# Kernel optimization log

Measured on AMD Instinct MI355X. Metric: run time of the kernel, lower is better.

The kernel has to match this reference:

```python
import jax, jax.numpy as jnp
import numpy as np

SOS = 1  # from init_kwargs

def gru_cell(x, h, W_ih, W_hh, b_ih, b_hh):
    # torch nn.GRU single-step cell semantics
    gi = x @ W_ih.T + b_ih            # [B, 3H]
    gh = h @ W_hh.T + b_hh            # [B, 3H]
    i_r, i_z, i_n = jnp.split(gi, 3, axis=-1)
    h_r, h_z, h_n = jnp.split(gh, 3, axis=-1)
    r = jax.nn.sigmoid(i_r + h_r)
    z = jax.nn.sigmoid(i_z + h_z)
    n = jnp.tanh(i_n + r * h_n)
    return (1.0 - z) * n + z * h

def setup_inputs() -> dict:
    key = jax.random.key(0)
    ks = jax.random.split(key, 12)
    V, E, H, L, B = 32000, 512, 512, 2, 32
    s = lambda k, shape: (jax.random.normal(k, shape, jnp.float32) * 0.05)
    return dict(
        h_0=s(ks[0], (L, B, H)),
        emb=s(ks[1], (V, E)),
        W_ih0=s(ks[2], (3 * H, E)), W_hh0=s(ks[3], (3 * H, H)),
        b_ih0=s(ks[4], (3 * H,)),   b_hh0=s(ks[5], (3 * H,)),
        W_ih1=s(ks[6], (3 * H, H)), W_hh1=s(ks[7], (3 * H, H)),
        b_ih1=s(ks[8], (3 * H,)),   b_hh1=s(ks[9], (3 * H,)),
        W_out=s(ks[10], (V, H)),    b_out=s(ks[11], (V,)),
        max_n=64,
    )

def reference(h_0, emb, W_ih0, W_hh0, b_ih0, b_hh0,
              W_ih1, W_hh1, b_ih1, b_hh1, W_out, b_out, max_n):
    B = h_0.shape[1]
    tok0 = jnp.full((B,), SOS, dtype=jnp.int32)

    def step(carry, _):
        h, tok = carry                              # h: [2, B, H], tok: [B]
        x = emb[tok]                                # [B, E] embedding gather
        h0n = gru_cell(x,   h[0], W_ih0, W_hh0, b_ih0, b_hh0)
        h1n = gru_cell(h0n, h[1], W_ih1, W_hh1, b_ih1, b_hh1)
        logits = h1n @ W_out.T + b_out              # [B, V]
        ntok = jnp.argmax(logits, axis=-1).astype(jnp.int32)
        return (jnp.stack([h0n, h1n]), ntok), ntok

    (h_t, _), toks = jax.lax.scan(step, (h_0, tok0), None, length=max_n)
    # toks: [max_n, B] -> [B, max_n] to mirror per-sequence output lists
    return toks.T, h_t
```

## Files before the change

kernel.cpp:

```cpp
#include <hip/hip_runtime.h>
#include <math.h>

#define NBLK 256
#define NTHR 512
#define Bsz  32
#define Hsz  512
#define Vsz  32000
#define BH   (Bsz*Hsz)
#define LDP  516
#define LDPB 520
#define CBLK 250
#define EPS  0.0045f

#define WS_HBUF   0
#define WS_PACKED 131072
#define WS_PLB    135168
#define WS_BAR    139264
#define WS_WPACK  143360
#define WS_WNORM  32911360
#define WS_CBAR   33039360
#define WS_NEEDED 33043456

#define PACKED_SEED 0x00000000FFFFFFFEull

typedef short short8 __attribute__((ext_vector_type(8)));
typedef float f32x4  __attribute__((ext_vector_type(4)));

struct Args {
  const float* h0_init;
  const float* emb;
  const float* Wih0; const float* Whh0; const float* bih0; const float* bhh0;
  const float* Wih1; const float* Whh1; const float* bih1; const float* bhh1;
  const float* Wout; const float* bout;
  const int*   maxn;
  float* out;
  float* hbuf;
  unsigned long long* packed;
  unsigned* plb;
  unsigned* bar;
  unsigned* cbar;
  const unsigned* wpack;
  const float* wnormE;
};

__device__ __forceinline__ unsigned short bf16_rne(float f){
  unsigned u = __float_as_uint(f);
  unsigned r = u + 0x7FFFu + ((u >> 16) & 1u);
  return (unsigned short)(r >> 16);
}
__device__ __forceinline__ float bf16v(float f){
  unsigned u = ((unsigned)bf16_rne(f)) << 16;
  return __uint_as_float(u);
}
__device__ __forceinline__ unsigned key32(float f){
  unsigned u = __float_as_uint(f);
  return (u & 0x80000000u) ? ~u : (u | 0x80000000u);
}

__device__ __forceinline__ unsigned long long cload8(const void* p){
  return __hip_atomic_load((const unsigned long long*)p,
                           __ATOMIC_RELAXED, __HIP_MEMORY_SCOPE_AGENT);
}
__device__ __forceinline__ unsigned cload4u(const unsigned* p){
  return __hip_atomic_load(p, __ATOMIC_RELAXED, __HIP_MEMORY_SCOPE_AGENT);
}
__device__ __forceinline__ void cstore4(float* p, float v){
  __hip_atomic_store(p, v, __ATOMIC_RELAXED, __HIP_MEMORY_SCOPE_AGENT);
}
__device__ __forceinline__ void cstore4u(unsigned* p, unsigned v){
  __hip_atomic_store(p, v, __ATOMIC_RELAXED, __HIP_MEMORY_SCOPE_AGENT);
}
__device__ __forceinline__ void cstore8(void* p, unsigned long long v){
  __hip_atomic_store((unsigned long long*)p, v,
                     __ATOMIC_RELAXED, __HIP_MEMORY_SCOPE_AGENT);
}

__device__ __forceinline__ short8 ntload8(const void* p){
  return __builtin_nontemporal_load((const short8*)p);
}

__device__ __forceinline__ void gridbar(unsigned* bar, int bid){
  __syncthreads();
  if (threadIdx.x == 0){
    asm volatile("s_waitcnt vmcnt(0)" ::: "memory");
    const int g = bid & 7;
    unsigned* gcnt = bar + g*32;
    unsigned* root = bar + 8*32;
    unsigned* gen  = bar + (9+g)*32;
    unsigned mygen = __hip_atomic_load(gen, __ATOMIC_RELAXED, __HIP_MEMORY_SCOPE_AGENT);
    unsigned go = __hip_atomic_fetch_add(gcnt, 1u, __ATOMIC_RELAXED, __HIP_MEMORY_SCOPE_AGENT);
    if (go == 31u){
      unsigned ro = __hip_atomic_fetch_add(root, 1u, __ATOMIC_RELAXED, __HIP_MEMORY_SCOPE_AGENT);
      if (ro == 7u){
        #pragma unroll
        for (int i = 0; i < 8; ++i)
          __hip_atomic_store(bar + i*32, 0u, __ATOMIC_RELAXED, __HIP_MEMORY_SCOPE_AGENT);
        __hip_atomic_store(root, 0u, __ATOMIC_RELAXED, __HIP_MEMORY_SCOPE_AGENT);
        asm volatile("s_waitcnt vmcnt(0)" ::: "memory");
        #pragma unroll
        for (int i = 0; i < 8; ++i)
          __hip_atomic_fetch_add(bar + (9+i)*32, 1u, __ATOMIC_RELAXED, __HIP_MEMORY_SCOPE_AGENT);
      }
    }
    while (__hip_atomic_load(gen, __ATOMIC_RELAXED, __HIP_MEMORY_SCOPE_AGENT) == mygen){
      __builtin_amdgcn_s_sleep(1);
    }
  }
  __syncthreads();
}

__device__ __forceinline__ void cluster_sync(unsigned* cnt, unsigned target){
  __syncthreads();
  if (threadIdx.x == 0){
    asm volatile("s_waitcnt vmcnt(0)" ::: "memory");
    __hip_atomic_fetch_add(cnt, 1u, __ATOMIC_RELAXED, __HIP_MEMORY_SCOPE_AGENT);
    while (__hip_atomic_load(cnt, __ATOMIC_RELAXED, __HIP_MEMORY_SCOPE_AGENT) < target){
      __builtin_amdgcn_s_sleep(1);
    }
  }
  __syncthreads();
}

__device__ __forceinline__ void stage_h16(const float* g, unsigned short* s16, int tid){
  const unsigned long long* gd = (const unsigned long long*)g;
  #pragma unroll
  for (int n = 0; n < 16; ++n){
    int idx = n*512 + tid;
    int row = idx >> 8;
    int col2 = idx & 255;
    unsigned long long v = __hip_atomic_load(gd + idx, __ATOMIC_RELAXED,
                                             __HIP_MEMORY_SCOPE_AGENT);
    unsigned short b0 = bf16_rne(__uint_as_float((unsigned)v));
    unsigned short b1 = bf16_rne(__uint_as_float((unsigned)(v >> 32)));
    *(unsigned*)&s16[row*LDPB + col2*2] = (unsigned)b0 | ((unsigned)b1 << 16);
  }
}

__device__ __forceinline__ void stage_h(const float* g, float* s, int tid){
  const unsigned long long* gd = (const unsigned long long*)g;
  #pragma unroll
  for (int n = 0; n < 16; ++n){
    int idx = n*512 + tid;
    int row = idx >> 8;
    int col = idx & 255;
    unsigned long long v = __hip_atomic_load(gd + idx, __ATOMIC_RELAXED,
                                             __HIP_MEMORY_SCOPE_AGENT);
    *(unsigned long long*)(s + row*LDP + col*2) = v;
  }
}

__device__ __forceinline__ void stage_row(const float* g, float* s, int tid){
  if (tid < 256){
    unsigned long long v = __hip_atomic_load((const unsigned long long*)g + tid,
                                             __ATOMIC_RELAXED, __HIP_MEMORY_SCOPE_AGENT);
    *(unsigned long long*)(s + tid*2) = v;
  }
}

__device__ __forceinline__ float red8(float v){
  v += __shfl_xor(v, 1); v += __shfl_xor(v, 2); v += __shfl_xor(v, 4);
  return v;
}
__device__ __forceinline__ float dot4acc(float4 w, float4 x, float acc){
  return fmaf(w.x,x.x, fmaf(w.y,x.y, fmaf(w.z,x.z, fmaf(w.w,x.w, acc))));
}

__device__ __forceinline__ void dot3(const float* row, const float* W, int j,
                                     int lane8, float& g0, float& g1, float& g2){
  const float* w = W + (size_t)j * Hsz;
  float a0 = 0.f, a1 = 0.f, a2 = 0.f;
  #pragma unroll 4
  for (int i = 0; i < 16; ++i){
    int k = i*32 + lane8*4;
    float4 v = *(const float4*)(row + k);
    a0 = dot4acc(*(const float4*)(w + k),            v, a0);
    a1 = dot4acc(*(const float4*)(w + 512*512 + k),  v, a1);
    a2 = dot4acc(*(const float4*)(w + 2*512*512 + k),v, a2);
  }
  g0 = red8(a0); g1 = red8(a1); g2 = red8(a2);
}

__device__ __forceinline__ void gru_oct(
    const float* xrow, const float* hrow,
    const float* Wih, const float* Whh,
    const float* bih, const float* bhh,
    int j, int lane8, float* hout_g)
{
  const float* wir = Wih + (size_t)j * Hsz;
  const float* whr = Whh + (size_t)j * Hsz;
  float ar=0.f, az=0.f, an=0.f, hr=0.f, hz=0.f, hn=0.f;
  #pragma unroll 4
  for (int i = 0; i < 16; ++i){
    int k = i*32 + lane8*4;
    float4 xv = *(const float4*)(xrow + k);
    float4 hv = *(const float4*)(hrow + k);
    ar = dot4acc(*(const float4*)(wir + k),            xv, ar);
    az = dot4acc(*(const float4*)(wir + 512*512 + k),  xv, az);
    an = dot4acc(*(const float4*)(wir + 2*512*512 + k),xv, an);
    hr = dot4acc(*(const float4*)(whr + k),            hv, hr);
    hz = dot4acc(*(const float4*)(whr + 512*512 + k),  hv, hz);
    hn = dot4acc(*(const float4*)(whr + 2*512*512 + k),hv, hn);
  }
  ar = red8(ar); az = red8(az); an = red8(an);
  hr = red8(hr); hz = red8(hz); hn = red8(hn);
  if (lane8 == 0){
    float r = 1.f/(1.f + expf(-(ar + bih[j]       + hr + bhh[j])));
    float z = 1.f/(1.f + expf(-(az + bih[Hsz+j]   + hz + bhh[Hsz+j])));
    float n = tanhf(an + bih[2*Hsz+j] + r*(hn + bhh[2*Hsz+j]));
    cstore4(hout_g, (1.f - z)*n + z*hrow[j]);
  }
}

__global__ __launch_bounds__(512) void repack_kernel(const float* __restrict__ Wout,
                                                     unsigned* __restrict__ wpack,
                                                     float* __restrict__ wnormE){
  const int rb = blockIdx.x;
  const int g = threadIdx.x >> 6;
  const int lane = threadIdx.x & 63;
  const int n = rb*128 + g*16 + (lane & 15);
  const int kq = (lane >> 4) * 8;
  float sumsq = 0.f;
  for (int c = 0; c < 16; ++c){
    const float* p = Wout + (size_t)n*512 + c*32 + kq;
    float4 f0 = *(const float4*)p;
    float4 f1 = *(const float4*)(p + 4);
    unsigned short s0 = bf16_rne(f0.x), s1 = bf16_rne(f0.y),
                   s2 = bf16_rne(f0.z), s3 = bf16_rne(f0.w),
                   s4 = bf16_rne(f1.x), s5 = bf16_rne(f1.y),
                   s6 = bf16_rne(f1.z), s7 = bf16_rne(f1.w);
    float v;
    v = __uint_as_float(((unsigned)s0)<<16); sumsq += v*v;
    v = __uint_as_float(((unsigned)s1)<<16); sumsq += v*v;
    v = __uint_as_float(((unsigned)s2)<<16); sumsq += v*v;
    v = __uint_as_float(((unsigned)s3)<<16); sumsq += v*v;
    v = __uint_as_float(((unsigned)s4)<<16); sumsq += v*v;
    v = __uint_as_float(((unsigned)s5)<<16); sumsq += v*v;
    v = __uint_as_float(((unsigned)s6)<<16); sumsq += v*v;
    v = __uint_as_float(((unsigned)s7)<<16); sumsq += v*v;
    uint4 u;
    u.x = (unsigned)s0 | ((unsigned)s1<<16);
    u.y = (unsigned)s2 | ((unsigned)s3<<16);
    u.z = (unsigned)s4 | ((unsigned)s5<<16);
    u.w = (unsigned)s6 | ((unsigned)s7<<16);
    *(uint4*)(wpack + (size_t)(((rb*8+g)*16 + c))*256 + lane*4) = u;
  }
  sumsq += __shfl_xor(sumsq, 16);
  sumsq += __shfl_xor(sumsq, 32);
  if (lane < 16) wnormE[n] = EPS * sqrtf(sumsq);
}

__global__ __launch_bounds__(NTHR, 1) void decoder_kernel(Args a){
  const int tid = threadIdx.x;
  const int bid = blockIdx.x;
  const int wave = tid >> 6;
  const int lane = tid & 63;
  const int b  = bid >> 3;
  const int s  = bid & 7;
  const int j0 = s * 64;
  const int T = a.maxn[0];
  float* h0g = a.hbuf;
  float* h1g = a.hbuf + BH;

  __shared__ __align__(16) unsigned short shB16[Bsz*LDPB];
  __shared__ float h0row[LDP];
  __shared__ float h1row[LDP];
  __shared__ float ghA[3][64];
  __shared__ float ghB[3][64];
  __shared__ float h0own[64];
  __shared__ float h1own[64];
  __shared__ unsigned lbmaxL[32];
  __shared__ unsigned maxlbL[32];
  __shared__ float hnormL[32];
  __shared__ int sh_tok0;
  __shared__ int candCnt;
  __shared__ int candList[512];
  __shared__ unsigned candUB[512];

  short8 bw[16];
  float bias = 0.f, wn = 0.f;
  if (bid < CBLK){
    const unsigned* wbase = a.wpack + (size_t)((bid*8 + wave)*16)*256 + lane*4;
    #pragma unroll
    for (int c = 0; c < 16; ++c){
      bw[c] = ntload8(wbase + c*256);
      asm volatile("" : "+a"(bw[c]));
    }
    int n = bid*128 + wave*16 + (lane & 15);
    bias = a.bout[n];
    wn = a.wnormE[n];
  }

  if (tid < 64){
    h0own[tid] = a.h0_init[(size_t)b*Hsz + j0 + tid];
    h1own[tid] = a.h0_init[BH + (size_t)b*Hsz + j0 + tid];
  }
  stage_row(a.h0_init + (size_t)b*Hsz, h0row, tid);
  stage_row(a.h0_init + BH + (size_t)b*Hsz, h1row, tid);
  __syncthreads();
  {
    int oct = tid >> 3, lane8 = tid & 7;
    int j = j0 + oct;
    float hr, hz, hn;  dot3(h0row, a.Whh0, j, lane8, hr, hz, hn);
    float kr, kz, kn;  dot3(h1row, a.Whh1, j, lane8, kr, kz, kn);
    if (lane8 == 0){
      ghA[0][oct] = hr; ghA[1][oct] = hz; ghA[2][oct] = hn;
      ghB[0][oct] = kr; ghB[1][oct] = kz; ghB[2][oct] = kn;
    }
  }
  __syncthreads();

  unsigned ctarget = 0;
  for (int t = 0; t < T; ++t){
    if (tid == 0){
      int tok = 1;
      if (t > 0){
        tok = (int)(~(unsigned)(cload8(&a.packed[b*16]) & 0xffffffffULL));
        if ((unsigned)tok >= (unsigned)Vsz) tok = 1;
      }
      sh_tok0 = tok;
    }
    __syncthreads();
    {
      int oct = tid >> 3, lane8 = tid & 7;
      int j = j0 + oct;
      const float* xrow = a.emb + (size_t)sh_tok0 * Hsz;
      float ar, az, an;  dot3(xrow, a.Wih0, j, lane8, ar, az, an);
      if (lane8 == 0){
        float hr = ghA[0][oct], hz = ghA[1][oct], hn = ghA[2][oct];
        float r = 1.f/(1.f + expf(-(ar + a.bih0[j]       + hr + a.bhh0[j])));
        float z = 1.f/(1.f + expf(-(az + a.bih0[Hsz+j]   + hz + a.bhh0[Hsz+j])));
        float n = tanhf(an + a.bih0[2*Hsz+j] + r*(hn + a.bhh0[2*Hsz+j]));
        float hnew = (1.f - z)*n + z*h0own[oct];
        cstore4(h0g + (size_t)b*Hsz + j, hnew);
        h0own[oct] = hnew;
      }
    }
    ctarget += 8;
    cluster_sync(a.cbar + b*32, ctarget);

    if (s == 0 && tid == 0){
      if (t > 0){
        unsigned long long p = cload8(&a.packed[b*16]);
        int tok = (int)(~(unsigned)(p & 0xffffffffULL));
        a.out[(size_t)b*T + (t-1)] = (float)tok;
      }
      cstore8(&a.packed[b*16], PACKED_SEED);
      cstore4u(&a.plb[b*32], 0u);
    }
    stage_row(h0g + (size_t)b*Hsz, h0row, tid);
    __syncthreads();
    {
      int oct = tid >> 3, lane8 = tid & 7;
      int j = j0 + oct;
      float ar, az, an;  dot3(h0row, a.Wih1, j, lane8, ar, az, an);
      if (lane8 == 0){
        float hr = ghB[0][oct], hz = ghB[1][oct], hn = ghB[2][oct];
        float r = 1.f/(1.f + expf(-(ar + a.bih1[j]       + hr + a.bhh1[j])));
        float z = 1.f/(1.f + expf(-(az + a.bih1[Hsz+j]   + hz + a.bhh1[Hsz+j])));
        float n = tanhf(an + a.bih1[2*Hsz+j] + r*(hn + a.bhh1[2*Hsz+j]));
        float hnew = (1.f - z)*n + z*h1own[oct];
        cstore4(h1g + (size_t)b*Hsz + j, hnew);
        h1own[oct] = hnew;
      }
    }
    gridbar(a.bar, bid);

    if (bid < CBLK) stage_h16(h1g, shB16, tid);
    stage_row(h1g + (size_t)b*Hsz, h1row, tid);
    if (tid < 32) lbmaxL[tid] = 0u;
    if (tid == 0) candCnt = 0;
    __syncthreads();
    {
      int oct = tid >> 3, lane8 = tid & 7;
      int j = j0 + oct;
      float hr, hz, hn;  dot3(h0row, a.Whh0, j, lane8, hr, hz, hn);
      float kr, kz, kn;  dot3(h1row, a.Whh1, j, lane8, kr, kz, kn);
      if (lane8 == 0){
        ghA[0][oct] = hr; ghA[1][oct] = hz; ghA[2][oct] = hn;
        ghB[0][oct] = kr; ghB[1][oct] = kz; ghB[2][oct] = kn;
      }
    }
    if (bid < CBLK){
      #pragma unroll
      for (int c = 0; c < 16; ++c) asm volatile("" : "+a"(bw[c]));

      if (tid < 256){
        int hb = tid >> 3, lane8 = tid & 7;
        float sq = 0.f;
        #pragma unroll
        for (int i = 0; i < 8; ++i){
          short8 sv = *(const short8*)&shB16[hb*LDPB + i*64 + lane8*8];
          #pragma unroll
          for (int q = 0; q < 8; ++q){
            float v = __uint_as_float(((unsigned)(unsigned short)sv[q]) << 16);
            sq = fmaf(v, v, sq);
          }
        }
        sq = red8(sq);
        if (lane8 == 0) hnormL[hb] = sqrtf(sq);
      }

      f32x4 accs[2];
      #pragma unroll
      for (int mt = 0; mt < 2; ++mt){
        f32x4 acc = {0.f, 0.f, 0.f, 0.f};
        const unsigned short* arow = shB16 + (mt*16 + (lane & 15))*LDPB + (lane >> 4)*8;
        #pragma unroll
        for (int c = 0; c < 16; ++c){
          short8 av = *(const short8*)(arow + c*32);
          acc = __builtin_amdgcn_mfma_f32_16x16x32_bf16(av, bw[c], acc, 0, 0, 0);
        }
        accs[mt] = acc;
      }
      __syncthreads();
      {
        int quad = lane >> 4;
        #pragma unroll
        for (int mt = 0; mt < 2; ++mt){
          #pragma unroll
          for (int r = 0; r < 4; ++r){
            int m = mt*16 + quad*4 + r;
            float lg = accs[mt][r] + bias;
            float lb = lg - wn * hnormL[m];
            unsigned lk = key32(lb), o;
            o = __shfl_xor(lk, 1); lk = lk > o ? lk : o;
            o = __shfl_xor(lk, 2); lk = lk > o ? lk : o;
            o = __shfl_xor(lk, 4); lk = lk > o ? lk : o;
            o = __shfl_xor(lk, 8); lk = lk > o ? lk : o;
            if ((lane & 15) == 0) atomicMax(&lbmaxL[m], lk);
          }
        }
      }
      __syncthreads();
      if (tid < 32) atomicMax(&a.plb[tid*32], lbmaxL[tid]);
      {
        int n_loc = wave*16 + (lane & 15);
        int quad = lane >> 4;
        #pragma unroll
        for (int mt = 0; mt < 2; ++mt){
          #pragma unroll
          for (int r = 0; r < 4; ++r){
            int m = mt*16 + quad*4 + r;
            float lg = accs[mt][r] + bias;
            float ub = lg + wn * hnormL[m];
            unsigned uk = key32(ub);
            if (uk >= lbmaxL[m]){
              int pos = atomicAdd(&candCnt, 1);
              if (pos < 512){ candList[pos] = n_loc*32 + m; candUB[pos] = uk; }
            }
          }
        }
      }
      __syncthreads();
      if (tid < 32){
        unsigned g = cload4u(&a.plb[tid*32]);
        unsigned l = lbmaxL[tid];
        maxlbL[tid] = g > l ? g : l;
      }
      __syncthreads();
      auto rescore = [&](int cidx, unsigned uk){
        int n_loc = cidx >> 5, rb = cidx & 31;
        if (uk < maxlbL[rb]) return;
        int n = bid*128 + n_loc;
        const float* wrow = a.Wout + (size_t)n*512 + lane*8;
        const unsigned long long* hq =
            (const unsigned long long*)(h1g + (size_t)rb*Hsz) + lane*4;
        unsigned long long q0 = cload8(hq),     q1 = cload8(hq + 1);
        unsigned long long q2 = cload8(hq + 2), q3 = cload8(hq + 3);
        float4 x0 = make_float4(__uint_as_float((unsigned)q0),
                                __uint_as_float((unsigned)(q0 >> 32)),
                                __uint_as_float((unsigned)q1),
                                __uint_as_float((unsigned)(q1 >> 32)));
        float4 x1 = make_float4(__uint_as_float((unsigned)q2),
                                __uint_as_float((unsigned)(q2 >> 32)),
                                __uint_as_float((unsigned)q3),
                                __uint_as_float((unsigned)(q3 >> 32)));
        float4 w0 = *(const float4*)wrow,      w1 = *(const float4*)(wrow + 4);
        float d = dot4acc(w0, x0, 0.f);
        d = dot4acc(w1, x1, d);
        d += __shfl_xor(d, 1);  d += __shfl_xor(d, 2);  d += __shfl_xor(d, 4);
        d += __shfl_xor(d, 8);  d += __shfl_xor(d, 16); d += __shfl_xor(d, 32);
        if (lane == 0){
          float lg = d + a.bout[n];
          unsigned long long key =
              (((unsigned long long)key32(lg)) << 32) | (unsigned)(~(unsigned)n);
          atomicMax(&a.packed[rb*16], key);
        }
      };
      int nc = candCnt;
      if (nc <= 512){
        for (int ci = wave; ci < nc; ci += 8) rescore(candList[ci], candUB[ci]);
      } else {
        for (int ci = wave; ci < 4096; ci += 8) rescore(ci, 0xFFFFFFFFu);
      }
    }
    gridbar(a.bar, bid);
  }

  if (bid == 0 && tid < Bsz){
    unsigned long long p = cload8(&a.packed[tid*16]);
    int tok = (int)(~(unsigned)(p & 0xffffffffULL));
    a.out[tid*T + (T-1)] = (float)tok;
  }
  int e = bid*NTHR + tid;
  if (e < BH/2){
    unsigned long long v0 = cload8((const unsigned long long*)h0g + e);
    unsigned long long v1 = cload8((const unsigned long long*)h1g + e);
    *((unsigned long long*)(a.out + Bsz*T) + e)      = v0;
    *((unsigned long long*)(a.out + Bsz*T + BH) + e) = v1;
  }
}

__global__ __launch_bounds__(NTHR, 1) void decoder_kernel_fb(Args a){
  const int tid = threadIdx.x;
  const int bid = blockIdx.x;
  const int T = a.maxn[0];
  float* h0g = a.hbuf;
  float* h1g = a.hbuf + BH;
  __shared__ float shA[Bsz*LDP];
  __shared__ float shB[Bsz*LDP];
  __shared__ unsigned long long lbest[32*32];
  __shared__ int sh_tok[Bsz];

  for (int t = 0; t < T; ++t){
    if (t == 0) stage_h(a.h0_init, shA, tid);
    if (tid < Bsz){
      int tok;
      if (t == 0) tok = 1;
      else {
        tok = (int)(~(unsigned)(cload8(&a.packed[tid*16]) & 0xffffffffULL));
        if ((unsigned)tok >= (unsigned)Vsz) tok = 1;
      }
      sh_tok[tid] = tok;
    }
    __syncthreads();
    {
      int oct = tid >> 3, lane8 = tid & 7;
      int b = oct & 31, jj = oct >> 5;
      int j = bid*2 + jj;
      const float* xrow = a.emb + (size_t)sh_tok[b] * Hsz;
      gru_oct(xrow, shA + b*LDP, a.Wih0, a.Whh0, a.bih0, a.bhh0,
              j, lane8, h0g + b*Hsz + j);
    }
    gridbar(a.bar, bid);
    if (bid == 0 && tid < Bsz){
      if (t > 0){
        unsigned long long p = cload8(&a.packed[tid*16]);
        a.out[tid*T + (t-1)] = (float)((int)(~(unsigned)(p & 0xffffffffULL)));
      }
      cstore8(&a.packed[tid*16], PACKED_SEED);
    }
    stage_h(h0g, shA, tid);
    if (t == 0) stage_h(a.h0_init + BH, shB, tid);
    __syncthreads();
    {
      int oct = tid >> 3, lane8 = tid & 7;
      int b = oct & 31, jj = oct >> 5;
      int j = bid*2 + jj;
      gru_oct(shA + b*LDP, shB + b*LDP, a.Wih1, a.Whh1, a.bih1, a.bhh1,
              j, lane8, h1g + b*Hsz + j);
    }
    gridbar(a.bar, bid);
    stage_h(h1g, shB, tid);
    __syncthreads();
    if (bid < CBLK){
      const int quad = tid >> 2, l4 = tid & 3;
      const int rg = quad & 31, bg = quad >> 5;
      const int rowbase = bid*128 + rg*4;
      const float* wr = a.Wout + (size_t)rowbase * Hsz;
      const float* hb = shB + bg*8*LDP;
      float acc[4][8];
      #pragma unroll
      for (int s = 0; s < 4; ++s)
        #pragma unroll
        for (int j = 0; j < 8; ++j) acc[s][j] = 0.f;
      #pragma unroll 2
      for (int i = 0; i < 32; ++i){
        const int k = i*16 + l4*4;
        float4 wv[4], hv[8];
        #pragma unroll
        for (int s = 0; s < 4; ++s) wv[s] = *(const float4*)(wr + (size_t)s*Hsz + k);
        #pragma unroll
        for (int j = 0; j < 8; ++j) hv[j] = *(const float4*)(hb + j*LDP + k);
        #pragma unroll
        for (int s = 0; s < 4; ++s)
          #pragma unroll
          for (int j = 0; j < 8; ++j) acc[s][j] = dot4acc(wv[s], hv[j], acc[s][j]);
      }
      #pragma unroll
      for (int s = 0; s < 4; ++s)
        #pragma unroll
        for (int j = 0; j < 8; ++j){
          float v = acc[s][j];
          v += __shfl_xor(v, 1); v += __shfl_xor(v, 2);
          acc[s][j] = v;
        }
      if (l4 == 0){
        float4 bv = *(const float4*)(a.bout + rowbase);
        float bb[4] = {bv.x, bv.y, bv.z, bv.w};
        #pragma unroll
        for (int j = 0; j < 8; ++j){
          float best = -3.4e38f; int bi = rowbase;
          #pragma unroll
          for (int s = 0; s < 4; ++s){
            float lv = acc[s][j] + bb[s];
            if (lv > best){ best = lv; bi = rowbase + s; }
          }
          unsigned u = __float_as_uint(best);
          unsigned key = (u & 0x80000000u) ? ~u : (u | 0x80000000u);
          lbest[rg*32 + bg*8 + j] =
              ((unsigned long long)key << 32) | (unsigned)(~(unsigned)bi);
        }
      }
      __syncthreads();
      if (tid < Bsz){
        unsigned long long m = lbest[tid];
        #pragma unroll 4
        for (int r = 1; r < 32; ++r){
          unsigned long long c = lbest[r*32 + tid];
          m = (c > m) ? c : m;
        }
        atomicMax(&a.packed[tid*16], m);
      }
    }
    gridbar(a.bar, bid);
  }
  if (bid == 0 && tid < Bsz){
    unsigned long long p = cload8(&a.packed[tid*16]);
    a.out[tid*T + (T-1)] = (float)((int)(~(unsigned)(p & 0xffffffffULL)));
  }
  int e = bid*NTHR + tid;
  if (e < BH/2){
    unsigned long long v0 = cload8((const unsigned long long*)h0g + e);
    unsigned long long v1 = cload8((const unsigned long long*)h1g + e);
    *((unsigned long long*)(a.out + Bsz*T) + e)      = v0;
    *((unsigned long long*)(a.out + Bsz*T + BH) + e) = v1;
  }
}

extern "C" void kernel_launch(void* const* d_in, const int* in_sizes, int n_in,
                              void* d_out, int out_size, void* d_ws, size_t ws_size,
                              hipStream_t stream){
  Args a;
  a.h0_init = (const float*)d_in[0];
  a.emb  = (const float*)d_in[1];
  a.Wih0 = (const float*)d_in[2];
  a.Whh0 = (const float*)d_in[3];
  a.bih0 = (const float*)d_in[4];
  a.bhh0 = (const float*)d_in[5];
  a.Wih1 = (const float*)d_in[6];
  a.Whh1 = (const float*)d_in[7];
  a.bih1 = (const float*)d_in[8];
  a.bhh1 = (const float*)d_in[9];
  a.Wout = (const float*)d_in[10];
  a.bout = (const float*)d_in[11];
  a.maxn = (const int*)d_in[12];
  a.out  = (float*)d_out;
  char* wsb = (char*)d_ws;
  a.hbuf   = (float*)(wsb + WS_HBUF);
  a.packed = (unsigned long long*)(wsb + WS_PACKED);
  a.plb    = (unsigned*)(wsb + WS_PLB);
  a.bar    = (unsigned*)(wsb + WS_BAR);
  a.cbar   = (unsigned*)(wsb + WS_CBAR);
  a.wpack  = (const unsigned*)(wsb + WS_WPACK);
  a.wnormE = (const float*)(wsb + WS_WNORM);

  hipMemsetAsync(wsb + WS_PACKED, 0, 12288, stream);

  void* params[] = { &a };
  if (ws_size >= (size_t)WS_NEEDED){
    hipMemsetAsync(wsb + WS_CBAR, 0, 4096, stream);
    repack_kernel<<<CBLK, 512, 0, stream>>>(a.Wout, (unsigned*)a.wpack, (float*)a.wnormE);
    hipLaunchCooperativeKernel((void*)decoder_kernel, dim3(NBLK), dim3(NTHR),
                               params, 0, stream);
  } else {
    hipLaunchCooperativeKernel((void*)decoder_kernel_fb, dim3(NBLK), dim3(NTHR),
                               params, 0, stream);
  }
}
```

Before: 2.598 ms.

## Replace grid-wide barriers with per-batch and per-group counter waits

Replaces the two grid-wide barriers per timestep with finer-grained dependency counters. A per-batch h1done counter signals when layer-1 hidden state is ready, and per-group rsc counters signal that the logits rescore phase is done. Blocks that only need their own batch row wait on one counter, while output-projection blocks wait on all 32, which lets independent blocks proceed without waiting on the whole grid. The cluster_sync also drops its explicit vmcnt wait, which risks memory-ordering hazards under the relaxed atomics.

New measurement: 2.677 ms. 3.0% more time.

```diff
diff --git a/kernel.cpp b/kernel.cpp
--- a/kernel.cpp
+++ b/kernel.cpp
@@ -19,7 +19,9 @@
 #define WS_WPACK  143360
 #define WS_WNORM  32911360
 #define WS_CBAR   33039360
-#define WS_NEEDED 33043456
+#define WS_H1D    33043456
+#define WS_RSC    33047552
+#define WS_NEEDED 33048576
 
 #define PACKED_SEED 0x00000000FFFFFFFEull
 
@@ -39,6 +41,8 @@
   unsigned* plb;
   unsigned* bar;
   unsigned* cbar;
+  unsigned* h1done;
+  unsigned* rsc;
   const unsigned* wpack;
   const float* wnormE;
 };
@@ -73,6 +77,9 @@
 __device__ __forceinline__ void cstore8(void* p, unsigned long long v){
   __hip_atomic_store((unsigned long long*)p, v,
                      __ATOMIC_RELAXED, __HIP_MEMORY_SCOPE_AGENT);
+}
+__device__ __forceinline__ void cincr(unsigned* p){
+  __hip_atomic_fetch_add(p, 1u, __ATOMIC_RELAXED, __HIP_MEMORY_SCOPE_AGENT);
 }
 
 __device__ __forceinline__ short8 ntload8(const void* p){
@@ -112,11 +119,30 @@
 __device__ __forceinline__ void cluster_sync(unsigned* cnt, unsigned target){
   __syncthreads();
   if (threadIdx.x == 0){
-    asm volatile("s_waitcnt vmcnt(0)" ::: "memory");
-    __hip_atomic_fetch_add(cnt, 1u, __ATOMIC_RELAXED, __HIP_MEMORY_SCOPE_AGENT);
+    cincr(cnt);
     while (__hip_atomic_load(cnt, __ATOMIC_RELAXED, __HIP_MEMORY_SCOPE_AGENT) < target){
       __builtin_amdgcn_s_sleep(1);
     }
+  }
+  __syncthreads();
+}
+
+__device__ __forceinline__ void wait_all32(unsigned* c, unsigned target, int tid){
+  if (tid < 32){
+    while (cload4u(c + tid*32) < target) __builtin_amdgcn_s_sleep(1);
+  }
+  __syncthreads();
+}
+__device__ __forceinline__ void wait_one(unsigned* c, unsigned target, int tid){
+  if (tid == 0){
+    while (cload4u(c) < target) __builtin_amdgcn_s_sleep(1);
+  }
+  __syncthreads();
+}
+__device__ __forceinline__ void wait_rsc(unsigned* rsc, unsigned tmul, int tid){
+  if (tid < 8){
+    unsigned cnt = (tid < 2) ? 32u : 31u;
+    while (cload4u(rsc + tid*32) < cnt*tmul) __builtin_amdgcn_s_sleep(1);
   }
   __syncthreads();
 }
@@ -311,6 +337,7 @@
 
   unsigned ctarget = 0;
   for (int t = 0; t < T; ++t){
+    wait_rsc(a.rsc, (unsigned)t, tid);
     if (tid == 0){
       int tok = 1;
       if (t > 0){
@@ -363,8 +390,12 @@
         h1own[oct] = hnew;
       }
     }
-    gridbar(a.bar, bid);
-
+    __syncthreads();
+    if (tid == 0) cincr(a.h1done + b*32);
+
+    unsigned h1target = 8u*(unsigned)(t+1);
+    if (bid < CBLK) wait_all32(a.h1done, h1target, tid);
+    else            wait_one(a.h1done + b*32, h1target, tid);
     if (bid < CBLK) stage_h16(h1g, shB16, tid);
     stage_row(h1g + (size_t)b*Hsz, h1row, tid);
     if (tid < 32) lbmaxL[tid] = 0u;
@@ -493,10 +524,12 @@
       } else {
         for (int ci = wave; ci < 4096; ci += 8) rescore(ci, 0xFFFFFFFFu);
       }
-    }
-    gridbar(a.bar, bid);
-  }
-
+      __syncthreads();
+      if (tid == 0) cincr(a.rsc + (bid & 7)*32);
+    }
+  }
+
+  wait_rsc(a.rsc, (unsigned)T, tid);
   if (bid == 0 && tid < Bsz){
     unsigned long long p = cload8(&a.packed[tid*16]);
     int tok = (int)(~(unsigned)(p & 0xffffffffULL));
@@ -662,6 +695,8 @@
   a.plb    = (unsigned*)(wsb + WS_PLB);
   a.bar    = (unsigned*)(wsb + WS_BAR);
   a.cbar   = (unsigned*)(wsb + WS_CBAR);
+  a.h1done = (unsigned*)(wsb + WS_H1D);
+  a.rsc    = (unsigned*)(wsb + WS_RSC);
   a.wpack  = (const unsigned*)(wsb + WS_WPACK);
   a.wnormE = (const float*)(wsb + WS_WNORM);
 
@@ -669,7 +704,7 @@
 
   void* params[] = { &a };
   if (ws_size >= (size_t)WS_NEEDED){
-    hipMemsetAsync(wsb + WS_CBAR, 0, 4096, stream);
+    hipMemsetAsync(wsb + WS_CBAR, 0, 9216, stream);
     repack_kernel<<<CBLK, 512, 0, stream>>>(a.Wout, (unsigned*)a.wpack, (float*)a.wnormE);
     hipLaunchCooperativeKernel((void*)decoder_kernel, dim3(NBLK), dim3(NTHR),
                                params, 0, stream);
```
